# Optimization experiments

Hardware: AMD Instinct MI355X
Metric: run time of the kernel (lower is better)

## Reference

```python
import jax, jax.numpy as jnp
import numpy as np
import math

B, T, C = 1, 2048, 2048
N_HEAD = 32
N_QUERY_GROUPS = 8
HEAD_SIZE = 64
ROPE_N_ELEM = 16  # int(0.25 * 64)
Q_PER_KV = N_HEAD // N_QUERY_GROUPS  # 4
QKV_DIM = (N_HEAD + 2 * N_QUERY_GROUPS) * HEAD_SIZE  # 3072


def setup_inputs() -> dict:
    key = jax.random.key(0)
    ks = jax.random.split(key, 7)
    x = jax.random.normal(ks[0], (B, T, C), dtype=jnp.float32)
    # realistic rope tables
    inv_freq = 1.0 / (10000.0 ** (jnp.arange(0, ROPE_N_ELEM, 2, dtype=jnp.float32) / ROPE_N_ELEM))
    t = jnp.arange(T, dtype=jnp.float32)
    freqs = jnp.outer(t, inv_freq)                       # [T, rope/2]
    emb = jnp.concatenate([freqs, freqs], axis=-1)       # [T, rope]
    cos, sin = jnp.cos(emb), jnp.sin(emb)
    s = 0.02
    W_attn = jax.random.normal(ks[1], (QKV_DIM, C), dtype=jnp.float32) * s
    b_attn = jax.random.normal(ks[2], (QKV_DIM,), dtype=jnp.float32) * s
    W_proj = jax.random.normal(ks[3], (C, N_HEAD * HEAD_SIZE), dtype=jnp.float32) * s
    b_proj = jax.random.normal(ks[4], (C,), dtype=jnp.float32) * s
    return {"x": x, "cos": cos, "sin": sin, "W_attn": W_attn, "b_attn": b_attn,
            "W_proj": W_proj, "b_proj": b_proj}


def _apply_rope(t, cos, sin):
    # t: [B, H, T, rope]; cos/sin: [T, rope]
    half = t.shape[-1] // 2
    t1, t2 = t[..., :half], t[..., half:]
    rotated = jnp.concatenate([-t2, t1], axis=-1)
    return t * cos + rotated * sin


def reference(x, cos, sin, W_attn, b_attn, W_proj, b_proj):
    Bc, Tc, Cc = x.shape
    qkv = x @ W_attn.T + b_attn                                   # [B, T, 3072]
    qkv = qkv.reshape(Bc, Tc, N_QUERY_GROUPS, Q_PER_KV + 2, HEAD_SIZE)
    qkv = qkv.transpose(0, 2, 3, 1, 4)                            # [B, G, q_per_kv+2, T, hs]
    q = qkv[:, :, :Q_PER_KV]                                      # [B, G, q_per_kv, T, hs]
    k = qkv[:, :, Q_PER_KV:Q_PER_KV + 1]                          # [B, G, 1, T, hs]
    v = qkv[:, :, Q_PER_KV + 1:]
    # GQA expand (n_query_groups != n_head, prefill path)
    k = jnp.broadcast_to(k, (Bc, N_QUERY_GROUPS, Q_PER_KV, Tc, HEAD_SIZE))
    v = jnp.broadcast_to(v, (Bc, N_QUERY_GROUPS, Q_PER_KV, Tc, HEAD_SIZE))
    q = q.reshape(Bc, N_HEAD, Tc, HEAD_SIZE)
    k = k.reshape(Bc, N_HEAD, Tc, HEAD_SIZE)
    v = v.reshape(Bc, N_HEAD, Tc, HEAD_SIZE)
    # partial RoPE on first ROPE_N_ELEM dims
    q = jnp.concatenate([_apply_rope(q[..., :ROPE_N_ELEM], cos, sin), q[..., ROPE_N_ELEM:]], axis=-1)
    k = jnp.concatenate([_apply_rope(k[..., :ROPE_N_ELEM], cos, sin), k[..., ROPE_N_ELEM:]], axis=-1)
    # causal SDPA with scale 1/sqrt(head_size)
    scale = 1.0 / math.sqrt(HEAD_SIZE)
    scores = jnp.einsum('bhqd,bhkd->bhqk', q, k) * scale          # [B, H, T, T]
    causal = jnp.tril(jnp.ones((Tc, Tc), dtype=bool))
    scores = jnp.where(causal, scores, jnp.finfo(scores.dtype).min)
    attn = jax.nn.softmax(scores, axis=-1)
    y = jnp.einsum('bhqk,bhkd->bhqd', attn, v)                    # [B, H, T, hs]
    y = y.transpose(0, 2, 1, 3).reshape(Bc, Tc, N_HEAD * HEAD_SIZE)
    return y @ W_proj.T + b_proj
```

## Files before the change

### kernel.cpp

```cpp
#include <hip/hip_runtime.h>
#include <hip/hip_bf16.h>

using u16 = unsigned short;
typedef float f32x4 __attribute__((ext_vector_type(4)));
typedef __bf16 bf16x8 __attribute__((ext_vector_type(8)));

#define T_SEQ 2048
#define C_DIM 2048
#define QKV_DIM 3072
#define N_HEAD 32
#define N_GROUPS 8
#define HEAD_SIZE 64
#define ROPE_N 16
#define NEG_BIG (-1e30f)
#define LSP 76
#define QSCALE 0.18033688011112043f

__device__ inline float bf2f(u16 u) {
    union { float f; unsigned v; } x; x.v = ((unsigned)u) << 16; return x.f;
}
__device__ inline u16 f2bf(float f) {
    __bf16 h = (__bf16)f;
    return *(u16*)&h;
}
__device__ inline int4 cvt8(int4 lo, int4 hi) {
    const float* fa = (const float*)&lo;
    const float* fb = (const float*)&hi;
    __attribute__((aligned(16))) u16 o[8] = {
        f2bf(fa[0]), f2bf(fa[1]), f2bf(fa[2]), f2bf(fa[3]),
        f2bf(fb[0]), f2bf(fb[1]), f2bf(fb[2]), f2bf(fb[3]) };
    return *(const int4*)o;
}

__device__ __forceinline__ int detect_fp32(const unsigned* __restrict__ xw) {
    int cnt = 0;
#pragma unroll
    for (int i = 0; i < 128; i++) {
        unsigned w = xw[i];
        cnt += (((w >> 7)  & 0xFF) >= 0xC0);
        cnt += (((w >> 23) & 0xFF) >= 0xC0);
    }
    return cnt > 8;
}

__device__ __forceinline__ void gl_lds16(const u16* g, u16* l) {
    __builtin_amdgcn_global_load_lds(
        (const __attribute__((address_space(1))) unsigned int*)g,
        (__attribute__((address_space(3))) unsigned int*)l,
        16, 0, 0);
}

struct ConvDesc {
    const void* src[7];
    u16*        dst[7];
    int         off8[8];
};

__global__ void convert_all(ConvDesc cd)
{
    const int fl = detect_fp32((const unsigned*)cd.src[0]);
    int gid = blockIdx.x * blockDim.x + threadIdx.x;
    if (gid >= cd.off8[7]) return;
    int seg = 0;
#pragma unroll
    for (int s = 1; s < 7; s++) seg += (gid >= cd.off8[s]);
    int i = (gid - cd.off8[seg]) * 8;
    if (fl) {
        const float4* s = (const float4*)((const float*)cd.src[seg] + i);
        *(int4*)(cd.dst[seg] + i) = cvt8(*(const int4*)&s[0], *(const int4*)&s[1]);
    } else {
        *(int4*)(cd.dst[seg] + i) = *(const int4*)((const u16*)cd.src[seg] + i);
    }
}

__global__ __launch_bounds__(256) void gemm_qkv_rope(
    const u16* __restrict__ A, const u16* __restrict__ W,
    const u16* __restrict__ bias,
    const u16* __restrict__ ccos, const u16* __restrict__ csin,
    u16* __restrict__ Qout, u16* __restrict__ Kout, u16* __restrict__ Vtout)
{
    __shared__ __attribute__((aligned(16))) u16 lds_a[2][64 * 64];
    __shared__ __attribute__((aligned(16))) u16 lds_b[2][128 * 64];

    const int tid  = threadIdx.x;
    const int wave = tid >> 6;
    const int lane = tid & 63;
    const int quad = lane >> 4;
    const int l16  = lane & 15;
    const int bm = blockIdx.y * 64;
    const int bn = blockIdx.x * 128;
    const int K = C_DIM;

    f32x4 acc[4][2] = {};

    int srow[4], sgc[4];
#pragma unroll
    for (int k = 0; k < 4; k++) {
        int s = tid + k * 256;
        srow[k] = s >> 3;
        sgc[k]  = (s & 7) ^ (srow[k] & 7);
    }
    const int xh = l16 & 7;

    auto stage = [&](int k0, int p) {
#pragma unroll
        for (int k = 0; k < 2; k++) {
            int s = tid + k * 256;
            gl_lds16(A + (size_t)(bm + srow[k]) * K + k0 + sgc[k] * 8, lds_a[p] + s * 8);
        }
#pragma unroll
        for (int k = 0; k < 4; k++) {
            int s = tid + k * 256;
            gl_lds16(W + (size_t)(bn + srow[k]) * K + k0 + sgc[k] * 8, lds_b[p] + s * 8);
        }
    };

    stage(0, 0);
    const int nsteps = K / 64;
    for (int kt = 0; kt < nsteps; kt++) {
        const int p = kt & 1;
        __syncthreads();
        if (kt + 1 < nsteps) stage((kt + 1) * 64, p ^ 1);

        bf16x8 afr[4][2], bfr[2][2];
#pragma unroll
        for (int ks = 0; ks < 2; ks++) {
            int c = ((ks * 4 + quad) ^ xh) * 8;
#pragma unroll
            for (int i = 0; i < 4; i++)
                afr[i][ks] = *(const bf16x8*)(lds_a[p] + (i * 16 + l16) * 64 + c);
#pragma unroll
            for (int j = 0; j < 2; j++)
                bfr[j][ks] = *(const bf16x8*)(lds_b[p] + (wave * 32 + j * 16 + l16) * 64 + c);
        }
#pragma unroll
        for (int ks = 0; ks < 2; ks++)
#pragma unroll
            for (int i = 0; i < 4; i++)
#pragma unroll
                for (int j = 0; j < 2; j++)
                    acc[i][j] = __builtin_amdgcn_mfma_f32_16x16x32_bf16(afr[i][ks], bfr[j][ks], acc[i][j], 0, 0, 0);
    }

#pragma unroll
    for (int j = 0; j < 2; j++) {
        const int colb = bn + wave * 32 + j * 16;
        const int col  = colb + l16;
        const int slot = (colb % 384) >> 6;
        const int g    = colb / 384;
        const int dbase = colb & 63;
        const int d    = dbase + l16;
        const float bv = bf2f(bias[col]);
        const bool rope = (dbase == 0) && (slot != 5);
#pragma unroll
        for (int i = 0; i < 4; i++) {
            const int trow = bm + i * 16 + quad * 4;
#pragma unroll
            for (int r = 0; r < 4; r++) {
                float v = acc[i][j][r] + bv;
                float outv = v;
                if (rope) {
                    float part = __shfl_xor(v, 8, 64);
                    float rot = (l16 < 8) ? -part : part;
                    float cc = bf2f(ccos[(trow + r) * ROPE_N + l16]);
                    float ss = bf2f(csin[(trow + r) * ROPE_N + l16]);
                    outv = v * cc + rot * ss;
                }
                const int t = trow + r;
                if (slot < 4) {
                    int hh = g * 4 + slot;
                    Qout[((size_t)hh * T_SEQ + t) * 64 + d] = f2bf(outv * QSCALE);
                } else if (slot == 4) {
                    Kout[((size_t)g * T_SEQ + t) * 64 + d] = f2bf(outv);
                } else {
                    Vtout[((size_t)g * 64 + d) * T_SEQ + t] = f2bf(outv);
                }
            }
        }
    }
}

__global__ __launch_bounds__(256) void gemm_bt(
    const u16* __restrict__ A, const u16* __restrict__ W,
    const u16* __restrict__ bias, u16* __restrict__ Cout,
    int M, int N, int K, const unsigned* __restrict__ xprobe)
{
    __shared__ __attribute__((aligned(16))) u16 lds_a[2][64 * 64];
    __shared__ __attribute__((aligned(16))) u16 lds_b[2][64 * 64];

    const int tid  = threadIdx.x;
    const int wave = tid >> 6;
    const int lane = tid & 63;
    const int quad = lane >> 4;
    const int l16  = lane & 15;
    const int bm = blockIdx.y * 64;
    const int bn = blockIdx.x * 64;
    const int fl = detect_fp32(xprobe);

    f32x4 acc[4] = {};

    int srow[2], sgc[2];
#pragma unroll
    for (int k = 0; k < 2; k++) {
        int s = tid + k * 256;
        srow[k] = s >> 3;
        sgc[k]  = (s & 7) ^ (srow[k] & 7);
    }
    const int xh = l16 & 7;

    auto stage = [&](int k0, int p) {
#pragma unroll
        for (int k = 0; k < 2; k++) {
            int s = tid + k * 256;
            gl_lds16(A + (size_t)(bm + srow[k]) * K + k0 + sgc[k] * 8, lds_a[p] + s * 8);
            gl_lds16(W + (size_t)(bn + srow[k]) * K + k0 + sgc[k] * 8, lds_b[p] + s * 8);
        }
    };

    stage(0, 0);
    const int nsteps = K / 64;
    for (int kt = 0; kt < nsteps; kt++) {
        const int p = kt & 1;
        __syncthreads();
        if (kt + 1 < nsteps) stage((kt + 1) * 64, p ^ 1);

        bf16x8 afr[4][2], bfr[2];
#pragma unroll
        for (int ks = 0; ks < 2; ks++) {
            int c = ((ks * 4 + quad) ^ xh) * 8;
#pragma unroll
            for (int i = 0; i < 4; i++)
                afr[i][ks] = *(const bf16x8*)(lds_a[p] + (i * 16 + l16) * 64 + c);
            bfr[ks] = *(const bf16x8*)(lds_b[p] + (wave * 16 + l16) * 64 + c);
        }
#pragma unroll
        for (int ks = 0; ks < 2; ks++)
#pragma unroll
            for (int i = 0; i < 4; i++)
                acc[i] = __builtin_amdgcn_mfma_f32_16x16x32_bf16(afr[i][ks], bfr[ks], acc[i], 0, 0, 0);
    }

    const int col = bn + wave * 16 + l16;
    const float bv = bf2f(bias[col]);
#pragma unroll
    for (int i = 0; i < 4; i++) {
        int row = bm + i * 16 + quad * 4;
#pragma unroll
        for (int r = 0; r < 4; r++) {
            float v = acc[i][r] + bv;
            size_t idx = (size_t)(row + r) * N + col;
            if (fl) ((float*)Cout)[idx] = v;
            else    Cout[idx] = f2bf(v);
        }
    }
}

__global__ __launch_bounds__(256) void flash_attn(
    const u16* __restrict__ Q, const u16* __restrict__ K,
    const u16* __restrict__ Vt, u16* __restrict__ Y)
{
    __shared__ __attribute__((aligned(16))) u16 lds_q[64 * 64];
    __shared__ __attribute__((aligned(16))) u16 lds_k[2][64 * 64];
    __shared__ __attribute__((aligned(16))) u16 lds_vt[2][64 * 64];
    __shared__ __attribute__((aligned(16))) u16 lds_p[4][16 * LSP];

    const int h  = blockIdx.y;
    const int g  = h >> 2;
    const int qt = 31 - blockIdx.x;
    const int q0 = qt * 64;
    const int tid  = threadIdx.x;
    const int wave = tid >> 6;
    const int lane = tid & 63;
    const int quad = lane >> 4;
    const int l16  = lane & 15;

    const u16* Qh = Q  + (size_t)h * T_SEQ * 64;
    const u16* Kg = K  + (size_t)g * T_SEQ * 64;
    const u16* Vg = Vt + (size_t)g * 64 * T_SEQ;

    int srow[2], sgc[2];
#pragma unroll
    for (int k = 0; k < 2; k++) {
        int s = tid + k * 256;
        srow[k] = s >> 3;
        sgc[k]  = (s & 7) ^ (srow[k] & 7);
    }
    const int xh = l16 & 7;

    bf16x8 vones;
#pragma unroll
    for (int i = 0; i < 8; i++) vones[i] = (__bf16)1.0f;

    auto stage = [&](int k0, int p) {
#pragma unroll
        for (int k = 0; k < 2; k++) {
            int s = tid + k * 256;
            gl_lds16(Kg + (size_t)(k0 + srow[k]) * 64 + sgc[k] * 8, lds_k[p] + s * 8);
            gl_lds16(Vg + (size_t)srow[k] * T_SEQ + k0 + sgc[k] * 8, lds_vt[p] + s * 8);
        }
    };

#pragma unroll
    for (int k = 0; k < 2; k++) {
        int s = tid + k * 256;
        gl_lds16(Qh + (size_t)(q0 + srow[k]) * 64 + sgc[k] * 8, lds_q + s * 8);
    }
    stage(0, 0);

    f32x4 o_acc[4] = {};
    f32x4 acc_l = {};
    bf16x8 a_q[2];
    bool q_loaded = false;

    for (int kt = 0; kt <= qt; kt++) {
        const int p = kt & 1;
        __syncthreads();
        if (kt < qt) stage((kt + 1) * 64, p ^ 1);

        if (!q_loaded) {
#pragma unroll
            for (int ks = 0; ks < 2; ks++)
                a_q[ks] = *(const bf16x8*)(lds_q + (wave * 16 + l16) * 64 + (((ks * 4 + quad) ^ xh) * 8));
            q_loaded = true;
        }

        f32x4 sc[4] = {};
#pragma unroll
        for (int ks = 0; ks < 2; ks++) {
            int c = ((ks * 4 + quad) ^ xh) * 8;
#pragma unroll
            for (int t = 0; t < 4; t++) {
                bf16x8 bk = *(const bf16x8*)(lds_k[p] + (t * 16 + l16) * 64 + c);
                sc[t] = __builtin_amdgcn_mfma_f32_16x16x32_bf16(a_q[ks], bk, sc[t], 0, 0, 0);
            }
        }

        if (kt == qt) {
            const int row_g = q0 + wave * 16 + quad * 4;
            const int k0 = kt * 64;
#pragma unroll
            for (int t = 0; t < 4; t++) {
                int col_g = k0 + t * 16 + l16;
#pragma unroll
                for (int r = 0; r < 4; r++)
                    if (col_g > row_g + r) sc[t][r] = NEG_BIG;
            }
        }

#pragma unroll
        for (int t = 0; t < 4; t++) {
            int colo = t * 16 + l16;
#pragma unroll
            for (int r = 0; r < 4; r++) {
                float pv = __builtin_amdgcn_exp2f(sc[t][r]);
                lds_p[wave][(quad * 4 + r) * LSP + colo] = f2bf(pv);
            }
        }

#pragma unroll
        for (int ks = 0; ks < 2; ks++) {
            int c = ((ks * 4 + quad) ^ xh) * 8;
            bf16x8 apf = *(const bf16x8*)(lds_p[wave] + l16 * LSP + ks * 32 + quad * 8);
#pragma unroll
            for (int t = 0; t < 4; t++) {
                bf16x8 bvf = *(const bf16x8*)(lds_vt[p] + (t * 16 + l16) * 64 + c);
                o_acc[t] = __builtin_amdgcn_mfma_f32_16x16x32_bf16(apf, bvf, o_acc[t], 0, 0, 0);
            }
            acc_l = __builtin_amdgcn_mfma_f32_16x16x32_bf16(apf, vones, acc_l, 0, 0, 0);
        }
    }

#pragma unroll
    for (int t = 0; t < 4; t++)
#pragma unroll
        for (int r = 0; r < 4; r++) {
            int row = q0 + wave * 16 + quad * 4 + r;
            int d   = t * 16 + l16;
            Y[(size_t)row * (N_HEAD * HEAD_SIZE) + h * 64 + d] = f2bf(o_acc[t][r] / acc_l[r]);
        }
}

extern "C" void kernel_launch(void* const* d_in, const int* in_sizes, int n_in,
                              void* d_out, int out_size, void* d_ws, size_t ws_size,
                              hipStream_t stream)
{
    u16* base = (u16*)d_ws;

    u16* cx   = base;
    u16* cWa  = cx  + (size_t)T_SEQ * C_DIM;
    u16* cba  = cWa + (size_t)QKV_DIM * C_DIM;
    u16* cWp  = cba + QKV_DIM;
    u16* cbp  = cWp + (size_t)C_DIM * C_DIM;
    u16* ccos = cbp + C_DIM;
    u16* csin = ccos + (size_t)T_SEQ * ROPE_N;
    u16* Qb   = csin + (size_t)T_SEQ * ROPE_N;
    u16* Kb   = Qb + (size_t)N_HEAD * T_SEQ * HEAD_SIZE;
    u16* Vtb  = Kb + (size_t)N_GROUPS * T_SEQ * HEAD_SIZE;
    u16* Yb   = Vtb + (size_t)N_GROUPS * T_SEQ * HEAD_SIZE;

    dim3 blk(256);

    ConvDesc cd;
    const int sizes[7] = { T_SEQ * C_DIM, T_SEQ * ROPE_N, T_SEQ * ROPE_N,
                           QKV_DIM * C_DIM, QKV_DIM, C_DIM * C_DIM, C_DIM };
    u16* dsts[7] = { cx, ccos, csin, cWa, cba, cWp, cbp };
    int acc8 = 0;
    for (int i = 0; i < 7; i++) {
        cd.src[i] = d_in[i];
        cd.dst[i] = dsts[i];
        cd.off8[i] = acc8;
        acc8 += sizes[i] / 8;
    }
    cd.off8[7] = acc8;
    convert_all<<<dim3((acc8 + 255) / 256), blk, 0, stream>>>(cd);

    gemm_qkv_rope<<<dim3(QKV_DIM / 128, T_SEQ / 64), blk, 0, stream>>>(
        cx, cWa, cba, ccos, csin, Qb, Kb, Vtb);
    flash_attn<<<dim3(T_SEQ / 64, N_HEAD), blk, 0, stream>>>(Qb, Kb, Vtb, Yb);
    gemm_bt<<<dim3(C_DIM / 64, T_SEQ / 64), blk, 0, stream>>>(
        Yb, cWp, cbp, (u16*)d_out, T_SEQ, C_DIM, N_HEAD * HEAD_SIZE,
        (const unsigned*)d_in[0]);
}
```

Before: 281.5 us.

## Pair causal query tiles per block and stage K/V through registers

Result: faster. 247.0 us (-12.2%).

```diff
diff --git a/kernel.cpp b/kernel.cpp
--- a/kernel.cpp
+++ b/kernel.cpp
@@ -266,118 +266,121 @@
 
     const int h  = blockIdx.y;
     const int g  = h >> 2;
-    const int qt = 31 - blockIdx.x;
-    const int q0 = qt * 64;
     const int tid  = threadIdx.x;
     const int wave = tid >> 6;
     const int lane = tid & 63;
     const int quad = lane >> 4;
     const int l16  = lane & 15;
+    const int NQT = T_SEQ / 64;
 
     const u16* Qh = Q  + (size_t)h * T_SEQ * 64;
     const u16* Kg = K  + (size_t)g * T_SEQ * 64;
     const u16* Vg = Vt + (size_t)g * 64 * T_SEQ;
 
-    int srow[2], sgc[2];
-#pragma unroll
-    for (int k = 0; k < 2; k++) {
-        int s = tid + k * 256;
-        srow[k] = s >> 3;
-        sgc[k]  = (s & 7) ^ (srow[k] & 7);
-    }
-    const int xh = l16 & 7;
+    const int srow = tid >> 3;
+    const int sgc  = (tid & 7) ^ (srow & 7);
+    const int xh   = l16 & 7;
 
     bf16x8 vones;
 #pragma unroll
     for (int i = 0; i < 8; i++) vones[i] = (__bf16)1.0f;
 
-    auto stage = [&](int k0, int p) {
+    int4 kr0, kr1, vr0, vr1;
+    auto load_tile = [&](int k0) {
+        kr0 = *(const int4*)(Kg + (size_t)(k0 + srow) * 64 + sgc * 8);
+        kr1 = *(const int4*)(Kg + (size_t)(k0 + srow + 32) * 64 + sgc * 8);
+        vr0 = *(const int4*)(Vg + (size_t)srow * T_SEQ + k0 + sgc * 8);
+        vr1 = *(const int4*)(Vg + (size_t)(srow + 32) * T_SEQ + k0 + sgc * 8);
+    };
+
+    for (int pass = 0; pass < 2; pass++) {
+        const int qt = pass ? (NQT - 1 - blockIdx.x) : blockIdx.x;
+        const int q0 = qt * 64;
+
+        __syncthreads();
 #pragma unroll
         for (int k = 0; k < 2; k++) {
             int s = tid + k * 256;
-            gl_lds16(Kg + (size_t)(k0 + srow[k]) * 64 + sgc[k] * 8, lds_k[p] + s * 8);
-            gl_lds16(Vg + (size_t)srow[k] * T_SEQ + k0 + sgc[k] * 8, lds_vt[p] + s * 8);
-        }
-    };
-
-#pragma unroll
-    for (int k = 0; k < 2; k++) {
-        int s = tid + k * 256;
-        gl_lds16(Qh + (size_t)(q0 + srow[k]) * 64 + sgc[k] * 8, lds_q + s * 8);
-    }
-    stage(0, 0);
-
-    f32x4 o_acc[4] = {};
-    f32x4 acc_l = {};
-    bf16x8 a_q[2];
-    bool q_loaded = false;
-
-    for (int kt = 0; kt <= qt; kt++) {
-        const int p = kt & 1;
+            int row = srow + k * 32;
+            *(int4*)(lds_q + s * 8) =
+                *(const int4*)(Qh + (size_t)(q0 + row) * 64 + sgc * 8);
+        }
         __syncthreads();
-        if (kt < qt) stage((kt + 1) * 64, p ^ 1);
-
-        if (!q_loaded) {
-#pragma unroll
-            for (int ks = 0; ks < 2; ks++)
-                a_q[ks] = *(const bf16x8*)(lds_q + (wave * 16 + l16) * 64 + (((ks * 4 + quad) ^ xh) * 8));
-            q_loaded = true;
-        }
-
-        f32x4 sc[4] = {};
-#pragma unroll
-        for (int ks = 0; ks < 2; ks++) {
-            int c = ((ks * 4 + quad) ^ xh) * 8;
+
+        bf16x8 a_q[2];
+#pragma unroll
+        for (int ks = 0; ks < 2; ks++)
+            a_q[ks] = *(const bf16x8*)(lds_q + (wave * 16 + l16) * 64 + (((ks * 4 + quad) ^ xh) * 8));
+
+        f32x4 o_acc[4] = {};
+        f32x4 acc_l = {};
+
+        load_tile(0);
+
+        for (int kt = 0; kt <= qt; kt++) {
+            const int p = kt & 1;
+            *(int4*)(lds_k[p]  + tid * 8)         = kr0;
+            *(int4*)(lds_k[p]  + (tid + 256) * 8) = kr1;
+            *(int4*)(lds_vt[p] + tid * 8)         = vr0;
+            *(int4*)(lds_vt[p] + (tid + 256) * 8) = vr1;
+            __syncthreads();
+            if (kt < qt) load_tile((kt + 1) * 64);
+
+            f32x4 sc[4] = {};
+#pragma unroll
+            for (int ks = 0; ks < 2; ks++) {
+                int c = ((ks * 4 + quad) ^ xh) * 8;
+#pragma unroll
+                for (int t = 0; t < 4; t++) {
+                    bf16x8 bk = *(const bf16x8*)(lds_k[p] + (t * 16 + l16) * 64 + c);
+                    sc[t] = __builtin_amdgcn_mfma_f32_16x16x32_bf16(a_q[ks], bk, sc[t], 0, 0, 0);
+                }
+            }
+
+            if (kt == qt) {
+                const int row_g = q0 + wave * 16 + quad * 4;
+                const int k0 = kt * 64;
+#pragma unroll
+                for (int t = 0; t < 4; t++) {
+                    int col_g = k0 + t * 16 + l16;
+#pragma unroll
+                    for (int r = 0; r < 4; r++)
+                        if (col_g > row_g + r) sc[t][r] = NEG_BIG;
+                }
+            }
+
 #pragma unroll
             for (int t = 0; t < 4; t++) {
-                bf16x8 bk = *(const bf16x8*)(lds_k[p] + (t * 16 + l16) * 64 + c);
-                sc[t] = __builtin_amdgcn_mfma_f32_16x16x32_bf16(a_q[ks], bk, sc[t], 0, 0, 0);
-            }
-        }
-
-        if (kt == qt) {
-            const int row_g = q0 + wave * 16 + quad * 4;
-            const int k0 = kt * 64;
-#pragma unroll
-            for (int t = 0; t < 4; t++) {
-                int col_g = k0 + t * 16 + l16;
-#pragma unroll
-                for (int r = 0; r < 4; r++)
-                    if (col_g > row_g + r) sc[t][r] = NEG_BIG;
-            }
-        }
-
-#pragma unroll
-        for (int t = 0; t < 4; t++) {
-            int colo = t * 16 + l16;
+                int colo = t * 16 + l16;
+#pragma unroll
+                for (int r = 0; r < 4; r++) {
+                    float pv = __builtin_amdgcn_exp2f(sc[t][r]);
+                    lds_p[wave][(quad * 4 + r) * LSP + colo] = f2bf(pv);
+                }
+            }
+
+#pragma unroll
+            for (int ks = 0; ks < 2; ks++) {
+                int c = ((ks * 4 + quad) ^ xh) * 8;
+                bf16x8 apf = *(const bf16x8*)(lds_p[wave] + l16 * LSP + ks * 32 + quad * 8);
+#pragma unroll
+                for (int t = 0; t < 4; t++) {
+                    bf16x8 bvf = *(const bf16x8*)(lds_vt[p] + (t * 16 + l16) * 64 + c);
+                    o_acc[t] = __builtin_amdgcn_mfma_f32_16x16x32_bf16(apf, bvf, o_acc[t], 0, 0, 0);
+                }
+                acc_l = __builtin_amdgcn_mfma_f32_16x16x32_bf16(apf, vones, acc_l, 0, 0, 0);
+            }
+        }
+
+#pragma unroll
+        for (int t = 0; t < 4; t++)
 #pragma unroll
             for (int r = 0; r < 4; r++) {
-                float pv = __builtin_amdgcn_exp2f(sc[t][r]);
-                lds_p[wave][(quad * 4 + r) * LSP + colo] = f2bf(pv);
-            }
-        }
-
-#pragma unroll
-        for (int ks = 0; ks < 2; ks++) {
-            int c = ((ks * 4 + quad) ^ xh) * 8;
-            bf16x8 apf = *(const bf16x8*)(lds_p[wave] + l16 * LSP + ks * 32 + quad * 8);
-#pragma unroll
-            for (int t = 0; t < 4; t++) {
-                bf16x8 bvf = *(const bf16x8*)(lds_vt[p] + (t * 16 + l16) * 64 + c);
-                o_acc[t] = __builtin_amdgcn_mfma_f32_16x16x32_bf16(apf, bvf, o_acc[t], 0, 0, 0);
-            }
-            acc_l = __builtin_amdgcn_mfma_f32_16x16x32_bf16(apf, vones, acc_l, 0, 0, 0);
-        }
-    }
-
-#pragma unroll
-    for (int t = 0; t < 4; t++)
-#pragma unroll
-        for (int r = 0; r < 4; r++) {
-            int row = q0 + wave * 16 + quad * 4 + r;
-            int d   = t * 16 + l16;
-            Y[(size_t)row * (N_HEAD * HEAD_SIZE) + h * 64 + d] = f2bf(o_acc[t][r] / acc_l[r]);
-        }
+                int row = q0 + wave * 16 + quad * 4 + r;
+                int d   = t * 16 + l16;
+                Y[(size_t)row * (N_HEAD * HEAD_SIZE) + h * 64 + d] = f2bf(o_acc[t][r] / acc_l[r]);
+            }
+    }
 }
 
 extern "C" void kernel_launch(void* const* d_in, const int* in_sizes, int n_in,
@@ -416,7 +419,7 @@
 
     gemm_qkv_rope<<<dim3(QKV_DIM / 128, T_SEQ / 64), blk, 0, stream>>>(
         cx, cWa, cba, ccos, csin, Qb, Kb, Vtb);
-    flash_attn<<<dim3(T_SEQ / 64, N_HEAD), blk, 0, stream>>>(Qb, Kb, Vtb, Yb);
+    flash_attn<<<dim3(T_SEQ / 128, N_HEAD), blk, 0, stream>>>(Qb, Kb, Vtb, Yb);
     gemm_bt<<<dim3(C_DIM / 64, T_SEQ / 64), blk, 0, stream>>>(
         Yb, cWp, cbp, (u16*)d_out, T_SEQ, C_DIM, N_HEAD * HEAD_SIZE,
         (const unsigned*)d_in[0]);
```
